# Kernel tuning notes

Measured on AMD Instinct MI355X. Metric: run time of the kernel, lower is better.

## Reference

```python
import jax, jax.numpy as jnp
from jax import lax
import numpy as np

B, NROI, WS, CH = 2, 1024, 5, 18
E = WS * WS            # embed_dim = 25
HID = E * CH           # hidden_dim = 450


def setup_inputs() -> dict:
    key = jax.random.key(0)
    ks = jax.random.split(key, 16)
    f32 = jnp.float32
    rn = lambda k, shape, s=0.05: jax.random.normal(k, shape, f32) * s
    inp = {}
    inp['feat_fv_raw'] = jax.random.normal(ks[0], (B, 128, 64, 512), f32)
    inp['feat_bev_raw'] = jax.random.normal(ks[1], (B, 512, 200, 176), f32)
    # rois: (x0, y0, z0, dx, dy, dz, theta) in KITTI-like ranges
    u = jax.random.uniform(ks[2], (B, NROI, 7), f32)
    inp['rois'] = jnp.stack([
        u[..., 0] * 70.4,            # x0 in [0, 70.4]
        u[..., 1] * 80.0 - 40.0,     # y0 in [-40, 40]
        u[..., 2] * 2.5 - 2.0,       # z0 in [-2, 0.5]
        1.0 + 3.0 * u[..., 3],       # dx
        1.0 + 3.0 * u[..., 4],       # dy
        0.5 + 1.5 * u[..., 5],       # dz
        u[..., 6] * np.pi], axis=-1) # theta
    # pre_roi_pros_fv / bev (conv3x3 -> BN(eval) -> ReLU -> conv1x1)
    inp['fv_w1'] = rn(ks[3], (18, 128, 3, 3)); inp['fv_b1'] = jnp.zeros(18, f32)
    inp['fv_gamma'] = jnp.ones(18, f32); inp['fv_beta'] = jnp.zeros(18, f32)
    inp['fv_mean'] = jnp.zeros(18, f32); inp['fv_var'] = jnp.ones(18, f32)
    inp['fv_w2'] = rn(ks[4], (18, 18, 1, 1)); inp['fv_b2'] = jnp.zeros(18, f32)
    inp['bev_w1'] = rn(ks[5], (18, 512, 3, 3)); inp['bev_b1'] = jnp.zeros(18, f32)
    inp['bev_gamma'] = jnp.ones(18, f32); inp['bev_beta'] = jnp.zeros(18, f32)
    inp['bev_mean'] = jnp.zeros(18, f32); inp['bev_var'] = jnp.ones(18, f32)
    inp['bev_w2'] = rn(ks[6], (18, 18, 1, 1)); inp['bev_b2'] = jnp.zeros(18, f32)
    # shared MultiHeadSelfAttention (embed_dim=25, num_heads=5)
    inp['Wq'] = rn(ks[7], (E, E), 0.2); inp['bq'] = jnp.zeros(E, f32)
    inp['Wk'] = rn(ks[8], (E, E), 0.2); inp['bk'] = jnp.zeros(E, f32)
    inp['Wv'] = rn(ks[9], (E, E), 0.2); inp['bv'] = jnp.zeros(E, f32)
    inp['Wf'] = rn(ks[10], (E, E), 0.2); inp['bf'] = jnp.zeros(E, f32)
    # classifier head: Conv2d(36,18,3,p=1), fc1(450->225), fc2(225->3)
    inp['conv_w'] = rn(ks[11], (18, 36, 3, 3)); inp['conv_b'] = jnp.zeros(18, f32)
    inp['fc1_w'] = rn(ks[12], (HID // 2, HID)); inp['fc1_b'] = jnp.zeros(HID // 2, f32)
    inp['fc2_w'] = rn(ks[13], (3, HID // 2)); inp['fc2_b'] = jnp.zeros(3, f32)
    return inp


def _conv2d(x, w, b):
    p = (w.shape[2] - 1) // 2
    out = lax.conv_general_dilated(x, w, (1, 1), [(p, p), (p, p)],
                                   dimension_numbers=('NCHW', 'OIHW', 'NCHW'))
    return out + b[None, :, None, None]


def _pre(x, w1, b1, g, be, mu, var, w2, b2):
    x = _conv2d(x, w1, b1)
    x = (x - mu[None, :, None, None]) * (g / jnp.sqrt(var + 1e-3))[None, :, None, None] + be[None, :, None, None]
    return _conv2d(jax.nn.relu(x), w2, b2)


def _gen_box(roi):
    x0, y0, z0, x, y, z, th = [roi[:, i] for i in range(7)]
    c, s = jnp.cos(th), jnp.sin(th)
    x1 = x0 - (y * c + x * s) / 2; x2 = x0 + (y * c + x * s) / 2
    y1 = y0 - (y * s + x * c) / 2; y2 = y0 + (y * s + x * c) / 2
    z1 = z0 - z / 2; z2 = z0 + z / 2
    return jnp.stack([z1, x1, z2, x2], 1), jnp.stack([y1, x1, y2, x2], 1)


def _grids(bbox, is_bev):
    t = jnp.linspace(0.0, 1.0, WS)
    gz = bbox[:, 0:1] + t[None, :] * (bbox[:, 2:3] - bbox[:, 0:1])  # [N,5]
    gx = bbox[:, 1:2] + t[None, :] * (bbox[:, 3:4] - bbox[:, 1:2])
    gz = gz / 40.0 if is_bev else (gz + 1.0) / 2.0
    gx = (gx - 35.2) / 35.2
    n = bbox.shape[0]
    GZ = jnp.broadcast_to(gz[:, :, None], (n, WS, WS))  # meshgrid 'ij'
    GX = jnp.broadcast_to(gx[:, None, :], (n, WS, WS))
    return jnp.stack([GZ, GX], -1)  # [...,0]=x(width) coord, [...,1]=y(height) coord


def _grid_sample_nearest(feat, grids):
    # feat [C,H,W]; grids [N,5,5,2]; matches torch grid_sample(nearest, align_corners=True, zeros)
    C, H, W = feat.shape
    ix = jnp.round((grids[..., 0] + 1.0) * 0.5 * (W - 1))
    iy = jnp.round((grids[..., 1] + 1.0) * 0.5 * (H - 1))
    valid = (ix >= 0) & (ix <= W - 1) & (iy >= 0) & (iy <= H - 1)
    ixc = jnp.clip(ix, 0, W - 1).astype(jnp.int32)
    iyc = jnp.clip(iy, 0, H - 1).astype(jnp.int32)
    out = feat[:, iyc, ixc]                       # [C,N,5,5]
    out = jnp.where(valid[None], out, 0.0)
    return jnp.transpose(out, (1, 0, 2, 3))       # [N,C,5,5]


def _mhsa(feat1, feat2, Wq, bq, Wk, bk, Wv, bv, Wf, bf, nh=WS):
    N, T, Ed = feat1.shape
    hd = Ed // nh
    heads = lambda x, W, b: (x @ W.T + b).reshape(N, T, nh, hd).transpose(0, 2, 1, 3)
    q, k, v = heads(feat2, Wq, bq), heads(feat1, Wk, bk), heads(feat2, Wv, bv)
    attn = jax.nn.softmax(jnp.einsum('nhqd,nhkd->nhqk', q, k) / jnp.sqrt(jnp.float32(hd)), axis=-1)
    av = jnp.einsum('nhqk,nhkd->nhqd', attn, v).transpose(0, 2, 1, 3).reshape(N, T, Ed)
    return av @ Wf.T + bf + feat1


def _classifier(bev, fv, Wq, bq, Wk, bk, Wv, bv, Wf, bf, conv_w, conv_b, fc1_w, fc1_b, fc2_w, fc2_b):
    N = bev.shape[0]
    x1 = _mhsa(bev, fv, Wq, bq, Wk, bk, Wv, bv, Wf, bf).reshape(N, CH, WS, WS)
    x2 = _mhsa(fv, bev, Wq, bq, Wk, bk, Wv, bv, Wf, bf).reshape(N, CH, WS, WS)
    x = jnp.concatenate([x1, x2], axis=1)
    x = _conv2d(x, conv_w, conv_b).reshape(N, HID)
    x = jax.nn.relu(x @ fc1_w.T + fc1_b)
    return x @ fc2_w.T + fc2_b


def _logits(feat_fv_raw, feat_bev_raw, rois, fv_w1, fv_b1, fv_gamma, fv_beta, fv_mean, fv_var, fv_w2, fv_b2,
            bev_w1, bev_b1, bev_gamma, bev_beta, bev_mean, bev_var, bev_w2, bev_b2,
            Wq, bq, Wk, bk, Wv, bv, Wf, bf, conv_w, conv_b, fc1_w, fc1_b, fc2_w, fc2_b):
    ffv = _pre(feat_fv_raw, fv_w1, fv_b1, fv_gamma, fv_beta, fv_mean, fv_var, fv_w2, fv_b2)
    fbev = _pre(feat_bev_raw, bev_w1, bev_b1, bev_gamma, bev_beta, bev_mean, bev_var, bev_w2, bev_b2)

    def per_sample(ffv1, fbev1, roi):
        bfv, bbev = _gen_box(roi)
        sfv = _grid_sample_nearest(ffv1, _grids(bfv, False)).reshape(-1, CH, E)
        sbev = _grid_sample_nearest(fbev1, _grids(bbev, True)).reshape(-1, CH, E)
        return _classifier(sbev, sfv, Wq, bq, Wk, bk, Wv, bv, Wf, bf,
                           conv_w, conv_b, fc1_w, fc1_b, fc2_w, fc2_b)

    return jax.vmap(per_sample)(ffv, fbev, rois)  # [B, NROI, 3]


def reference(feat_fv_raw, feat_bev_raw, rois, fv_w1, fv_b1, fv_gamma, fv_beta, fv_mean, fv_var, fv_w2, fv_b2,
              bev_w1, bev_b1, bev_gamma, bev_beta, bev_mean, bev_var, bev_w2, bev_b2,
              Wq, bq, Wk, bk, Wv, bv, Wf, bf, conv_w, conv_b, fc1_w, fc1_b, fc2_w, fc2_b):
    logits = _logits(feat_fv_raw, feat_bev_raw, rois, fv_w1, fv_b1, fv_gamma, fv_beta, fv_mean, fv_var,
                     fv_w2, fv_b2, bev_w1, bev_b1, bev_gamma, bev_beta, bev_mean, bev_var, bev_w2, bev_b2,
                     Wq, bq, Wk, bk, Wv, bv, Wf, bf, conv_w, conv_b, fc1_w, fc1_b, fc2_w, fc2_b)
    preds = jnp.argmax(logits, axis=-1) + 1          # cls_pred per batch sample
    scores = jax.nn.softmax(logits, axis=-1)          # box_scores per batch sample
    return preds, scores
```

## Files before the change

### kernel.cpp

```cpp
#include <hip/hip_runtime.h>
#include <math.h>

__global__ void transpose_w_kernel(const float* __restrict__ w, float* __restrict__ wt, int C) {
  int idx = blockIdx.x * blockDim.x + threadIdx.x;
  int total = 18 * C * 9;
  if (idx >= total) return;
  int co = idx / (C * 9);
  int rem = idx % (C * 9);
  int ci = rem / 9;
  int tap = rem % 9;
  wt[(ci * 9 + tap) * 18 + co] = w[idx];
}

__global__ void transpose_fc1_kernel(const float* __restrict__ w, float* __restrict__ wt) {
  int idx = blockIdx.x * blockDim.x + threadIdx.x;
  if (idx >= 225 * 450) return;
  int o = idx / 450;
  int i = idx % 450;
  wt[i * 256 + o] = w[idx];
}

__global__ __launch_bounds__(512) void pre_merged_kernel(
    const float* __restrict__ xF, const float* __restrict__ wtF,
    const float* __restrict__ b1F, const float* __restrict__ gF,
    const float* __restrict__ beF, const float* __restrict__ muF,
    const float* __restrict__ vF, const float* __restrict__ w2F,
    const float* __restrict__ b2F, float* __restrict__ outF,
    const float* __restrict__ xB, const float* __restrict__ wtB,
    const float* __restrict__ b1B, const float* __restrict__ gB,
    const float* __restrict__ beB, const float* __restrict__ muB,
    const float* __restrict__ vB, const float* __restrict__ w2B,
    const float* __restrict__ b2B, float* __restrict__ outB) {
  int orig = blockIdx.x;
  int flat;
  if (orig < 1200) {
    flat = (orig & 7) * 150 + (orig >> 3);
  } else {
    int j = orig - 1200;
    flat = 1200 + (j & 7) * 128 + (j >> 3);
  }

  const float *x, *wt, *b1, *gamma, *beta, *mean, *var, *w2, *b2;
  float* out;
  int H, W, cs, xt, h, b;
  if (flat < 1200) {
    xt = flat % 3; h = (flat / 3) % 200; b = flat / 600;
    x = xB; wt = wtB; b1 = b1B; gamma = gB; beta = beB; mean = muB; var = vB;
    w2 = w2B; b2 = b2B; out = outB;
    H = 200; W = 176; cs = 64;
  } else {
    int f = flat - 1200;
    xt = f & 7; h = (f >> 3) & 63; b = f >> 9;
    x = xF; wt = wtF; b1 = b1F; gamma = gF; beta = beF; mean = muF; var = vF;
    w2 = w2F; b2 = b2F; out = outF;
    H = 64; W = 512; cs = 16;
  }

  int tid = threadIdx.x;
  int pixel = tid & 63;
  int split = __builtin_amdgcn_readfirstlane(tid >> 6);
  int w = xt * 64 + pixel;
  bool active = (w < W);

  float acc[18];
#pragma unroll
  for (int i = 0; i < 18; i++) acc[i] = 0.f;

  const float* xb = x + (size_t)b * (cs * 8) * H * W;
  int ci0 = split * cs;
  for (int ci = 0; ci < cs; ci++) {
    const float* plane = xb + (size_t)(ci0 + ci) * H * W;
#pragma unroll
    for (int dh = 0; dh < 3; dh++) {
      int r = h + dh - 1;
      if ((unsigned)r < (unsigned)H) {
        const float* row = plane + (size_t)r * W;
        float v0 = (active && w >= 1) ? row[w - 1] : 0.f;
        float v1 = active ? row[w] : 0.f;
        float v2 = (active && w + 1 < W) ? row[w + 1] : 0.f;
        const float* wp = wt + ((size_t)(ci0 + ci) * 9 + dh * 3) * 18;
#pragma unroll
        for (int co = 0; co < 18; co++) acc[co] = fmaf(v0, wp[co], acc[co]);
#pragma unroll
        for (int co = 0; co < 18; co++) acc[co] = fmaf(v1, wp[18 + co], acc[co]);
#pragma unroll
        for (int co = 0; co < 18; co++) acc[co] = fmaf(v2, wp[36 + co], acc[co]);
      }
    }
  }

  __shared__ float red[7][64][19];
  if (split > 0) {
#pragma unroll
    for (int co = 0; co < 18; co++) red[split - 1][pixel][co] = acc[co];
  }
  __syncthreads();
  if (split == 0 && active) {
#pragma unroll
    for (int s = 0; s < 7; s++)
#pragma unroll
      for (int co = 0; co < 18; co++) acc[co] += red[s][pixel][co];
    float y[18];
#pragma unroll
    for (int co = 0; co < 18; co++) {
      float sc = gamma[co] / sqrtf(var[co] + 1e-3f);
      y[co] = fmaxf((acc[co] + b1[co] - mean[co]) * sc + beta[co], 0.f);
    }
    size_t obase = (size_t)b * 18 * H * W + (size_t)h * W + w;
#pragma unroll
    for (int co2 = 0; co2 < 18; co2++) {
      float s2 = b2[co2];
#pragma unroll
      for (int c = 0; c < 18; c++) s2 = fmaf(y[c], w2[co2 * 18 + c], s2);
      out[obase + (size_t)co2 * H * W] = s2;
    }
  }
}

__global__ __launch_bounds__(256) void classifier_kernel(
    const float* __restrict__ ffv, const float* __restrict__ fbev,
    const float* __restrict__ rois, const float* __restrict__ Wq,
    const float* __restrict__ bq, const float* __restrict__ Wk,
    const float* __restrict__ bk, const float* __restrict__ Wv,
    const float* __restrict__ bv, const float* __restrict__ Wf,
    const float* __restrict__ bf, const float* __restrict__ conv_w,
    const float* __restrict__ conv_b, const float* __restrict__ wt_fc1,
    const float* __restrict__ fc1_b, const float* __restrict__ fc2_w,
    const float* __restrict__ fc2_b, float* __restrict__ out) {
  int rid = blockIdx.x;
  int b = rid >> 10;
  int tid = threadIdx.x;

  __shared__ __align__(16) float sW[4 * 25 * 28];
  __shared__ float sB[100];
  __shared__ __align__(16) float sfv[18 * 28], sbev[18 * 28];
  __shared__ __align__(16) float pr[6 * 18 * 28];
  __shared__ __align__(16) float av[2 * 18 * 28];
  __shared__ __align__(16) float xx[2 * 18 * 28];
  __shared__ __align__(16) float hid[452];
  __shared__ float h1r[226];
  __shared__ float lg[3];
  __shared__ int c_ixf[25], c_iyf[25], c_vf[25];
  __shared__ int c_ixb[25], c_iyb[25], c_vb[25];

  for (int t = tid; t < 625; t += 256) {
    int j = t / 25, i = t % 25;
    sW[(0 * 25 + j) * 28 + i] = Wq[t];
    sW[(1 * 25 + j) * 28 + i] = Wk[t];
    sW[(2 * 25 + j) * 28 + i] = Wv[t];
    sW[(3 * 25 + j) * 28 + i] = Wf[t];
  }
  if (tid < 25) {
    sB[tid] = bq[tid];
    sB[25 + tid] = bk[tid];
    sB[50 + tid] = bv[tid];
    sB[75 + tid] = bf[tid];
  }

  if (tid < 25) {
    const float* roi = rois + (size_t)rid * 7;
    double x0 = roi[0], y0 = roi[1], z0 = roi[2];
    double dx = roi[3], dy = roi[4], dz = roi[5], th = roi[6];
    double c = cos(th), s = sin(th);
    double half1 = (dy * c + dx * s) / 2.0;
    double half2 = (dy * s + dx * c) / 2.0;
    double bx1 = x0 - half1, bx2 = x0 + half1;
    double by1 = y0 - half2, by2 = y0 + half2;
    double bz1 = z0 - dz / 2.0, bz2 = z0 + dz / 2.0;
    int i = tid / 5, j = tid % 5;
    double ti = i * 0.25, tj = j * 0.25;
    double gz = bz1 + ti * (bz2 - bz1);
    gz = (gz + 1.0) / 2.0;
    double gx = bx1 + tj * (bx2 - bx1);
    gx = (gx - 35.2) / 35.2;
    double ixf = rint((gz + 1.0) * 0.5 * 511.0);
    double iyf = rint((gx + 1.0) * 0.5 * 63.0);
    c_vf[tid] = (ixf >= 0.0) && (ixf <= 511.0) && (iyf >= 0.0) && (iyf <= 63.0);
    c_ixf[tid] = (int)fmin(fmax(ixf, 0.0), 511.0);
    c_iyf[tid] = (int)fmin(fmax(iyf, 0.0), 63.0);
    double gzb = (by1 + ti * (by2 - by1)) / 40.0;
    double ixb = rint((gzb + 1.0) * 0.5 * 175.0);
    double iyb = rint((gx + 1.0) * 0.5 * 199.0);
    c_vb[tid] = (ixb >= 0.0) && (ixb <= 175.0) && (iyb >= 0.0) && (iyb <= 199.0);
    c_ixb[tid] = (int)fmin(fmax(ixb, 0.0), 175.0);
    c_iyb[tid] = (int)fmin(fmax(iyb, 0.0), 199.0);
  }
  __syncthreads();

  {
    const float* fvb = ffv + (size_t)b * 18 * 64 * 512;
    const float* bvb = fbev + (size_t)b * 18 * 200 * 176;
    for (int item = tid; item < 900; item += 256) {
      if (item < 450) {
        int ch = item / 25, pos = item % 25;
        sfv[ch * 28 + pos] = c_vf[pos] ? fvb[((size_t)ch * 64 + c_iyf[pos]) * 512 + c_ixf[pos]] : 0.f;
      } else {
        int it = item - 450;
        int ch = it / 25, pos = it % 25;
        sbev[ch * 28 + pos] = c_vb[pos] ? bvb[((size_t)ch * 200 + c_iyb[pos]) * 176 + c_ixb[pos]] : 0.f;
      }
    }
  }
  __syncthreads();

  for (int idx = tid; idx < 450; idx += 256) {
    int t = idx / 25, j = idx % 25;
    const float4* xa4 = (const float4*)(sfv + t * 28);
    const float4* xb4 = (const float4*)(sbev + t * 28);
    const float4* wq4 = (const float4*)(sW + (0 * 25 + j) * 28);
    const float4* wk4 = (const float4*)(sW + (1 * 25 + j) * 28);
    const float4* wv4 = (const float4*)(sW + (2 * 25 + j) * 28);
    float aqf = sB[j], akf = sB[25 + j], avf = sB[50 + j];
    float aqb = sB[j], akb = sB[25 + j], avb = sB[50 + j];
#pragma unroll
    for (int k = 0; k < 6; k++) {
      float4 xa = xa4[k], xb = xb4[k];
      float4 wq = wq4[k], wk = wk4[k], wv = wv4[k];
      aqf = fmaf(xa.w, wq.w, fmaf(xa.z, wq.z, fmaf(xa.y, wq.y, fmaf(xa.x, wq.x, aqf))));
      akf = fmaf(xa.w, wk.w, fmaf(xa.z, wk.z, fmaf(xa.y, wk.y, fmaf(xa.x, wk.x, akf))));
      avf = fmaf(xa.w, wv.w, fmaf(xa.z, wv.z, fmaf(xa.y, wv.y, fmaf(xa.x, wv.x, avf))));
      aqb = fmaf(xb.w, wq.w, fmaf(xb.z, wq.z, fmaf(xb.y, wq.y, fmaf(xb.x, wq.x, aqb))));
      akb = fmaf(xb.w, wk.w, fmaf(xb.z, wk.z, fmaf(xb.y, wk.y, fmaf(xb.x, wk.x, akb))));
      avb = fmaf(xb.w, wv.w, fmaf(xb.z, wv.z, fmaf(xb.y, wv.y, fmaf(xb.x, wv.x, avb))));
    }
    {
      float xa = sfv[t * 28 + 24], xb = sbev[t * 28 + 24];
      float wq = sW[(0 * 25 + j) * 28 + 24], wk = sW[(1 * 25 + j) * 28 + 24],
            wv = sW[(2 * 25 + j) * 28 + 24];
      aqf = fmaf(xa, wq, aqf); akf = fmaf(xa, wk, akf); avf = fmaf(xa, wv, avf);
      aqb = fmaf(xb, wq, aqb); akb = fmaf(xb, wk, akb); avb = fmaf(xb, wv, avb);
    }
    pr[(0 * 18 + t) * 28 + j] = aqf;
    pr[(1 * 18 + t) * 28 + j] = akf;
    pr[(2 * 18 + t) * 28 + j] = avf;
    pr[(3 * 18 + t) * 28 + j] = aqb;
    pr[(4 * 18 + t) * 28 + j] = akb;
    pr[(5 * 18 + t) * 28 + j] = avb;
  }
  __syncthreads();

  const float rs5 = 0.44721359549995793f;
  if (tid < 90) {
    int hh = tid / 18, t = tid % 18;
#pragma unroll
    for (int m = 0; m < 2; m++) {
      const float* q = pr + (m == 0 ? 0 : 3) * 18 * 28;
      const float* k = pr + (m == 0 ? 4 : 1) * 18 * 28;
      const float* v = pr + (m == 0 ? 2 : 5) * 18 * 28;
      float p_[18];
      float mx = -1e30f;
#pragma unroll
      for (int ss = 0; ss < 18; ss++) {
        float sc = 0.f;
#pragma unroll
        for (int d = 0; d < 5; d++)
          sc = fmaf(q[t * 28 + hh * 5 + d], k[ss * 28 + hh * 5 + d], sc);
        sc *= rs5;
        p_[ss] = sc;
        mx = fmaxf(mx, sc);
      }
      float sm = 0.f;
#pragma unroll
      for (int ss = 0; ss < 18; ss++) {
        p_[ss] = expf(p_[ss] - mx);
        sm += p_[ss];
      }
      float inv = 1.f / sm;
#pragma unroll
      for (int d = 0; d < 5; d++) {
        float a = 0.f;
#pragma unroll
        for (int ss = 0; ss < 18; ss++)
          a = fmaf(p_[ss], v[ss * 28 + hh * 5 + d], a);
        av[(m * 18 + t) * 28 + hh * 5 + d] = a * inv;
      }
    }
  }
  __syncthreads();

  for (int idx = tid; idx < 450; idx += 256) {
    int t = idx / 25, j = idx % 25;
    const float4* wf4 = (const float4*)(sW + (3 * 25 + j) * 28);
    const float4* a04 = (const float4*)(av + (0 * 18 + t) * 28);
    const float4* a14 = (const float4*)(av + (1 * 18 + t) * 28);
    float s1 = sB[75 + j] + sbev[t * 28 + j];
    float s2 = sB[75 + j] + sfv[t * 28 + j];
#pragma unroll
    for (int k = 0; k < 6; k++) {
      float4 wf = wf4[k], a0 = a04[k], a1 = a14[k];
      s1 = fmaf(a0.w, wf.w, fmaf(a0.z, wf.z, fmaf(a0.y, wf.y, fmaf(a0.x, wf.x, s1))));
      s2 = fmaf(a1.w, wf.w, fmaf(a1.z, wf.z, fmaf(a1.y, wf.y, fmaf(a1.x, wf.x, s2))));
    }
    {
      float wf = sW[(3 * 25 + j) * 28 + 24];
      s1 = fmaf(av[(0 * 18 + t) * 28 + 24], wf, s1);
      s2 = fmaf(av[(1 * 18 + t) * 28 + 24], wf, s2);
    }
    xx[(0 * 18 + t) * 28 + j] = s1;
    xx[(1 * 18 + t) * 28 + j] = s2;
  }
  __syncthreads();

  for (int idx = tid; idx < 450; idx += 256) {
    int co = idx / 25, pos = idx % 25, pi = pos / 5, pj = pos % 5;
    float acc = conv_b[co];
    for (int ci = 0; ci < 36; ci++) {
      const float* xc = (ci < 18) ? &xx[(0 * 18 + ci) * 28] : &xx[(1 * 18 + (ci - 18)) * 28];
      const float* wp = conv_w + ((size_t)co * 36 + ci) * 9;
#pragma unroll
      for (int dh = 0; dh < 3; dh++) {
        int rr = pi + dh - 1;
        if ((unsigned)rr < 5u) {
#pragma unroll
          for (int dw = 0; dw < 3; dw++) {
            int cc = pj + dw - 1;
            if ((unsigned)cc < 5u) acc = fmaf(xc[rr * 5 + cc], wp[dh * 3 + dw], acc);
          }
        }
      }
    }
    hid[idx] = acc;
  }
  __syncthreads();

  if (tid < 225) {
    int o = tid;
    float a0 = fc1_b[o], a1 = 0.f, a2 = 0.f, a3 = 0.f;
    const float4* h4 = (const float4*)hid;
    for (int k = 0; k < 112; k++) {
      float4 hv = h4[k];
      int i = k * 4;
      a0 = fmaf(hv.x, wt_fc1[(size_t)i * 256 + o], a0);
      a1 = fmaf(hv.y, wt_fc1[(size_t)(i + 1) * 256 + o], a1);
      a2 = fmaf(hv.z, wt_fc1[(size_t)(i + 2) * 256 + o], a2);
      a3 = fmaf(hv.w, wt_fc1[(size_t)(i + 3) * 256 + o], a3);
    }
    a0 = fmaf(hid[448], wt_fc1[(size_t)448 * 256 + o], a0);
    a1 = fmaf(hid[449], wt_fc1[(size_t)449 * 256 + o], a1);
    h1r[o] = fmaxf((a0 + a1) + (a2 + a3), 0.f);
  }
  __syncthreads();

  int wave = tid >> 6, lane = tid & 63;
  if (wave < 3) {
    const float* wr = fc2_w + (size_t)wave * 225;
    float p = 0.f;
#pragma unroll
    for (int k = 0; k < 4; k++) {
      int i = lane + k * 64;
      if (i < 225) p = fmaf(h1r[i], wr[i], p);
    }
#pragma unroll
    for (int m = 32; m >= 1; m >>= 1) p += __shfl_xor(p, m);
    if (lane == 0) lg[wave] = p + fc2_b[wave];
  }
  __syncthreads();

  if (tid == 0) {
    float l0 = lg[0], l1 = lg[1], l2 = lg[2];
    int arg = 0;
    float bm = l0;
    if (l1 > bm) { arg = 1; bm = l1; }
    if (l2 > bm) { arg = 2; bm = l2; }
    float m = fmaxf(l0, fmaxf(l1, l2));
    float e0 = expf(l0 - m), e1 = expf(l1 - m), e2 = expf(l2 - m);
    float inv = 1.f / (e0 + e1 + e2);
    out[rid] = (float)(arg + 1);
    float* sc = out + 2048 + (size_t)rid * 3;
    sc[0] = e0 * inv;
    sc[1] = e1 * inv;
    sc[2] = e2 * inv;
  }
}

extern "C" void kernel_launch(void* const* d_in, const int* in_sizes, int n_in,
                              void* d_out, int out_size, void* d_ws, size_t ws_size,
                              hipStream_t stream) {
  const float* feat_fv = (const float*)d_in[0];
  const float* feat_bev = (const float*)d_in[1];
  const float* rois = (const float*)d_in[2];
  const float* fv_w1 = (const float*)d_in[3];
  const float* fv_b1 = (const float*)d_in[4];
  const float* fv_gamma = (const float*)d_in[5];
  const float* fv_beta = (const float*)d_in[6];
  const float* fv_mean = (const float*)d_in[7];
  const float* fv_var = (const float*)d_in[8];
  const float* fv_w2 = (const float*)d_in[9];
  const float* fv_b2 = (const float*)d_in[10];
  const float* bev_w1 = (const float*)d_in[11];
  const float* bev_b1 = (const float*)d_in[12];
  const float* bev_gamma = (const float*)d_in[13];
  const float* bev_beta = (const float*)d_in[14];
  const float* bev_mean = (const float*)d_in[15];
  const float* bev_var = (const float*)d_in[16];
  const float* bev_w2 = (const float*)d_in[17];
  const float* bev_b2 = (const float*)d_in[18];
  const float* Wq = (const float*)d_in[19];
  const float* bq = (const float*)d_in[20];
  const float* Wk = (const float*)d_in[21];
  const float* bk = (const float*)d_in[22];
  const float* Wv = (const float*)d_in[23];
  const float* bv = (const float*)d_in[24];
  const float* Wf = (const float*)d_in[25];
  const float* bf = (const float*)d_in[26];
  const float* conv_w = (const float*)d_in[27];
  const float* conv_b = (const float*)d_in[28];
  const float* fc1_w = (const float*)d_in[29];
  const float* fc1_b = (const float*)d_in[30];
  const float* fc2_w = (const float*)d_in[31];
  const float* fc2_b = (const float*)d_in[32];

  float* ws = (float*)d_ws;
  float* ffv = ws;
  float* fbev = ffv + 1179648;
  float* wt_fv = fbev + 1267200;
  float* wt_bev = wt_fv + 20736;
  float* wt_fc1 = wt_bev + 82944;

  transpose_w_kernel<<<(18 * 128 * 9 + 255) / 256, 256, 0, stream>>>(fv_w1, wt_fv, 128);
  transpose_w_kernel<<<(18 * 512 * 9 + 255) / 256, 256, 0, stream>>>(bev_w1, wt_bev, 512);
  transpose_fc1_kernel<<<(225 * 450 + 255) / 256, 256, 0, stream>>>(fc1_w, wt_fc1);

  pre_merged_kernel<<<2224, 512, 0, stream>>>(
      feat_fv, wt_fv, fv_b1, fv_gamma, fv_beta, fv_mean, fv_var, fv_w2, fv_b2, ffv,
      feat_bev, wt_bev, bev_b1, bev_gamma, bev_beta, bev_mean, bev_var, bev_w2, bev_b2, fbev);

  classifier_kernel<<<2048, 256, 0, stream>>>(
      ffv, fbev, rois, Wq, bq, Wk, bk, Wv, bv, Wf, bf, conv_w, conv_b, wt_fc1,
      fc1_b, fc2_w, fc2_b, (float*)d_out);
}
```

Before: 387.9 us.

## Compute two output rows per block in merged conv3x3 kernel to reuse weights

```diff
diff --git a/kernel.cpp b/kernel.cpp
--- a/kernel.cpp
+++ b/kernel.cpp
@@ -33,24 +33,24 @@
     const float* __restrict__ b2B, float* __restrict__ outB) {
   int orig = blockIdx.x;
   int flat;
-  if (orig < 1200) {
-    flat = (orig & 7) * 150 + (orig >> 3);
+  if (orig < 600) {
+    flat = (orig & 7) * 75 + (orig >> 3);
   } else {
-    int j = orig - 1200;
-    flat = 1200 + (j & 7) * 128 + (j >> 3);
+    int j = orig - 600;
+    flat = 600 + (j & 7) * 64 + (j >> 3);
   }
 
   const float *x, *wt, *b1, *gamma, *beta, *mean, *var, *w2, *b2;
   float* out;
   int H, W, cs, xt, h, b;
-  if (flat < 1200) {
-    xt = flat % 3; h = (flat / 3) % 200; b = flat / 600;
+  if (flat < 600) {
+    xt = flat % 3; h = 2 * ((flat / 3) % 100); b = flat / 300;
     x = xB; wt = wtB; b1 = b1B; gamma = gB; beta = beB; mean = muB; var = vB;
     w2 = w2B; b2 = b2B; out = outB;
     H = 200; W = 176; cs = 64;
   } else {
-    int f = flat - 1200;
-    xt = f & 7; h = (f >> 3) & 63; b = f >> 9;
+    int f = flat - 600;
+    xt = f & 7; h = 2 * ((f >> 3) & 31); b = f >> 8;
     x = xF; wt = wtF; b1 = b1F; gamma = gF; beta = beF; mean = muF; var = vF;
     w2 = w2F; b2 = b2F; out = outF;
     H = 64; W = 512; cs = 16;
@@ -62,9 +62,9 @@
   int w = xt * 64 + pixel;
   bool active = (w < W);
 
-  float acc[18];
-#pragma unroll
-  for (int i = 0; i < 18; i++) acc[i] = 0.f;
+  float acc[18], acc2[18];
+#pragma unroll
+  for (int i = 0; i < 18; i++) { acc[i] = 0.f; acc2[i] = 0.f; }
 
   const float* xb = x + (size_t)b * (cs * 8) * H * W;
   int ci0 = split * cs;
@@ -72,13 +72,13 @@
     const float* plane = xb + (size_t)(ci0 + ci) * H * W;
 #pragma unroll
     for (int dh = 0; dh < 3; dh++) {
+      const float* wp = wt + ((size_t)(ci0 + ci) * 9 + dh * 3) * 18;
       int r = h + dh - 1;
       if ((unsigned)r < (unsigned)H) {
         const float* row = plane + (size_t)r * W;
         float v0 = (active && w >= 1) ? row[w - 1] : 0.f;
         float v1 = active ? row[w] : 0.f;
         float v2 = (active && w + 1 < W) ? row[w + 1] : 0.f;
-        const float* wp = wt + ((size_t)(ci0 + ci) * 9 + dh * 3) * 18;
 #pragma unroll
         for (int co = 0; co < 18; co++) acc[co] = fmaf(v0, wp[co], acc[co]);
 #pragma unroll
@@ -86,10 +86,24 @@
 #pragma unroll
         for (int co = 0; co < 18; co++) acc[co] = fmaf(v2, wp[36 + co], acc[co]);
       }
+      int r2 = h + dh;
+      if ((unsigned)r2 < (unsigned)H) {
+        const float* row2 = plane + (size_t)r2 * W;
+        float u0 = (active && w >= 1) ? row2[w - 1] : 0.f;
+        float u1 = active ? row2[w] : 0.f;
+        float u2 = (active && w + 1 < W) ? row2[w + 1] : 0.f;
+#pragma unroll
+        for (int co = 0; co < 18; co++) acc2[co] = fmaf(u0, wp[co], acc2[co]);
+#pragma unroll
+        for (int co = 0; co < 18; co++) acc2[co] = fmaf(u1, wp[18 + co], acc2[co]);
+#pragma unroll
+        for (int co = 0; co < 18; co++) acc2[co] = fmaf(u2, wp[36 + co], acc2[co]);
+      }
     }
   }
 
   __shared__ float red[7][64][19];
+
   if (split > 0) {
 #pragma unroll
     for (int co = 0; co < 18; co++) red[split - 1][pixel][co] = acc[co];
@@ -107,6 +121,33 @@
       y[co] = fmaxf((acc[co] + b1[co] - mean[co]) * sc + beta[co], 0.f);
     }
     size_t obase = (size_t)b * 18 * H * W + (size_t)h * W + w;
+#pragma unroll
+    for (int co2 = 0; co2 < 18; co2++) {
+      float s2 = b2[co2];
+#pragma unroll
+      for (int c = 0; c < 18; c++) s2 = fmaf(y[c], w2[co2 * 18 + c], s2);
+      out[obase + (size_t)co2 * H * W] = s2;
+    }
+  }
+  __syncthreads();
+
+  if (split > 0) {
+#pragma unroll
+    for (int co = 0; co < 18; co++) red[split - 1][pixel][co] = acc2[co];
+  }
+  __syncthreads();
+  if (split == 0 && active) {
+#pragma unroll
+    for (int s = 0; s < 7; s++)
+#pragma unroll
+      for (int co = 0; co < 18; co++) acc2[co] += red[s][pixel][co];
+    float y[18];
+#pragma unroll
+    for (int co = 0; co < 18; co++) {
+      float sc = gamma[co] / sqrtf(var[co] + 1e-3f);
+      y[co] = fmaxf((acc2[co] + b1[co] - mean[co]) * sc + beta[co], 0.f);
+    }
+    size_t obase = (size_t)b * 18 * H * W + (size_t)(h + 1) * W + w;
 #pragma unroll
     for (int co2 = 0; co2 < 18; co2++) {
       float s2 = b2[co2];
@@ -421,7 +462,7 @@
   transpose_w_kernel<<<(18 * 512 * 9 + 255) / 256, 256, 0, stream>>>(bev_w1, wt_bev, 512);
   transpose_fc1_kernel<<<(225 * 450 + 255) / 256, 256, 0, stream>>>(fc1_w, wt_fc1);
 
-  pre_merged_kernel<<<2224, 512, 0, stream>>>(
+  pre_merged_kernel<<<1112, 512, 0, stream>>>(
       feat_fv, wt_fv, fv_b1, fv_gamma, fv_beta, fv_mean, fv_var, fv_w2, fv_b2, ffv,
       feat_bev, wt_bev, bev_b1, bev_gamma, bev_beta, bev_mean, bev_var, bev_w2, bev_b2, fbev);
 
```

Measured after the change: 390.9 us. Within noise of the previous version (+0.8%).
